# Kernel optimization log

Measured on AMD Instinct MI355X. Metric: run time of the kernel, lower is better.

The kernel has to match this reference:

```python
import jax, jax.numpy as jnp
import numpy as np

EMBED = 1024
HEADS = 16
HDIM = 64
FFN = 4 * EMBED
EPS = 1e-5


def setup_inputs() -> dict:
    key = jax.random.key(0)
    ks = jax.random.split(key, 12)
    def lin(k, fan_in, shape):
        b = 1.0 / np.sqrt(fan_in)
        return jax.random.uniform(k, shape, jnp.float32, -b, b)
    return {
        "x": jax.random.normal(ks[0], (4, 2048, EMBED), jnp.float32),
        "Wq": lin(ks[1], EMBED, (EMBED, HEADS * HDIM)),
        "Wk": lin(ks[2], EMBED, (EMBED, HEADS * HDIM)),
        "Wv": lin(ks[3], EMBED, (EMBED, HEADS * HDIM)),
        "Wo": lin(ks[4], HEADS * HDIM, (HEADS * HDIM, EMBED)),
        "ln1_g": jnp.ones((EMBED,), jnp.float32),
        "ln1_b": jnp.zeros((EMBED,), jnp.float32),
        "ln2_g": jnp.ones((EMBED,), jnp.float32),
        "ln2_b": jnp.zeros((EMBED,), jnp.float32),
        "W1": lin(ks[5], EMBED, (EMBED, FFN)),
        "b1": lin(ks[6], EMBED, (FFN,)),
        "W2": lin(ks[7], FFN, (FFN, EMBED)),
        "b2": lin(ks[8], FFN, (EMBED,)),
    }


def _layer_norm(x, g, b):
    mu = jnp.mean(x, axis=-1, keepdims=True)
    var = jnp.var(x, axis=-1, keepdims=True)
    return (x - mu) * jax.lax.rsqrt(var + EPS) * g + b


def reference(x, Wq, Wk, Wv, Wo, ln1_g, ln1_b, ln2_g, ln2_b, W1, b1, W2, b2):
    B, S, _ = x.shape
    residual = x
    h = _layer_norm(x, ln1_g, ln1_b)
    # project and split heads: [B, H, S, Dh]
    q = (h @ Wq).reshape(B, S, HEADS, HDIM).transpose(0, 2, 1, 3)
    k = (h @ Wk).reshape(B, S, HEADS, HDIM).transpose(0, 2, 1, 3)
    v = (h @ Wv).reshape(B, S, HEADS, HDIM).transpose(0, 2, 1, 3)
    scale = HDIM ** -0.5
    scores = jnp.einsum("bhqd,bhkd->bhqk", q, k) * scale
    # causal mask (upper triangle excluded above diagonal -> -inf)
    mask = jnp.triu(jnp.ones((S, S), bool), k=1)
    scores = jnp.where(mask, -jnp.inf, scores)
    attn = jax.nn.softmax(scores, axis=-1)
    out = jnp.einsum("bhqk,bhkd->bhqd", attn, v)
    out = out.transpose(0, 2, 1, 3).reshape(B, S, HEADS * HDIM)
    x = residual + out @ Wo
    residual = x
    h = _layer_norm(x, ln2_g, ln2_b)
    h = jax.nn.gelu(h @ W1 + b1, approximate=False) @ W2 + b2
    return residual + h
```

## Files before the change

### kernel.cpp

```cpp
#include <hip/hip_runtime.h>
#include <hip/hip_bf16.h>
#include <math.h>

typedef __bf16 bf16;
typedef bf16 bf16x8 __attribute__((ext_vector_type(8)));
typedef bf16 bf16x4 __attribute__((ext_vector_type(4)));
typedef float f32x4 __attribute__((ext_vector_type(4)));

#define ROWS 8192
#define EMB  1024
#define NH   16
#define HD   64
#define FFN  4096
#define QKVN 3072
#define SEQ  2048

__device__ __forceinline__ void gl2lds16(const bf16* g, bf16* l) {
  __builtin_amdgcn_global_load_lds((const __attribute__((address_space(1))) void*)g,
                                   (__attribute__((address_space(3))) void*)l, 16, 0, 0);
}

__global__ void transpose_cast(const float* __restrict__ W, bf16* __restrict__ Wt,
                               int K, int N, float scale) {
  __shared__ float tile[32][33];
  const int n0 = blockIdx.x * 32, k0 = blockIdx.y * 32;
  const int tx = threadIdx.x & 31, ty = threadIdx.x >> 5;
#pragma unroll
  for (int i = 0; i < 32; i += 8)
    tile[ty + i][tx] = W[(size_t)(k0 + ty + i) * N + n0 + tx];
  __syncthreads();
#pragma unroll
  for (int i = 0; i < 32; i += 8)
    Wt[(size_t)(n0 + ty + i) * K + k0 + tx] = (bf16)(tile[tx][ty + i] * scale);
}

__global__ void v_transpose(const bf16* __restrict__ qkv, bf16* __restrict__ vt) {
  __shared__ bf16 tile[32][33];
  const int s0 = blockIdx.x * 32, d0 = blockIdx.y * 32, bh = blockIdx.z;
  const int b = bh >> 4, h = bh & 15;
  const int tx = threadIdx.x & 31, ty = threadIdx.x >> 5;
#pragma unroll
  for (int i = 0; i < 32; i += 8)
    tile[ty + i][tx] = qkv[(size_t)(b * SEQ + s0 + ty + i) * QKVN + 2 * EMB + h * HD + d0 + tx];
  __syncthreads();
#pragma unroll
  for (int i = 0; i < 32; i += 8)
    vt[(size_t)(bh * HD + d0 + ty + i) * SEQ + s0 + tx] = tile[tx][ty + i];
}

__global__ void layernorm_bf16(const float* __restrict__ x, const float* __restrict__ g,
                               const float* __restrict__ b, bf16* __restrict__ out) {
  const int row = blockIdx.x;
  const int t = threadIdx.x;
  const float4 v = ((const float4*)(x + (size_t)row * EMB))[t];
  float s = v.x + v.y + v.z + v.w;
  float ss = v.x * v.x + v.y * v.y + v.z * v.z + v.w * v.w;
#pragma unroll
  for (int off = 32; off; off >>= 1) {
    s += __shfl_down(s, off);
    ss += __shfl_down(ss, off);
  }
  __shared__ float sbuf[8];
  const int wave = t >> 6, lane = t & 63;
  if (lane == 0) { sbuf[wave] = s; sbuf[4 + wave] = ss; }
  __syncthreads();
  if (t == 0) {
    float S = sbuf[0] + sbuf[1] + sbuf[2] + sbuf[3];
    float SS = sbuf[4] + sbuf[5] + sbuf[6] + sbuf[7];
    float mu = S * (1.0f / EMB);
    float var = SS * (1.0f / EMB) - mu * mu;
    sbuf[0] = mu;
    sbuf[1] = rsqrtf(var + 1e-5f);
  }
  __syncthreads();
  const float mu = sbuf[0], rs = sbuf[1];
  const float4 gv = ((const float4*)g)[t];
  const float4 bv = ((const float4*)b)[t];
  bf16x4 o;
  o[0] = (bf16)((v.x - mu) * rs * gv.x + bv.x);
  o[1] = (bf16)((v.y - mu) * rs * gv.y + bv.y);
  o[2] = (bf16)((v.z - mu) * rs * gv.z + bv.z);
  o[3] = (bf16)((v.w - mu) * rs * gv.w + bv.w);
  *(bf16x4*)(out + (size_t)row * EMB + t * 4) = o;
}

template <int EPI, int N_, int K_>
__global__ __launch_bounds__(256, 2) void gemm_bt(
    const bf16* __restrict__ A, const bf16* __restrict__ Bt, void* __restrict__ C,
    const float* __restrict__ bias, const float* __restrict__ resid) {
  constexpr int N = N_, K = K_;
  __shared__ __align__(16) bf16 As[128 * 64];
  __shared__ __align__(16) bf16 Bs[128 * 64];
  const int tid = threadIdx.x;
  const int lane = tid & 63;
  const int wave = tid >> 6;
  const int wm = (wave >> 1) * 64;
  const int wn = (wave & 1) * 64;
  constexpr int tn = N / 128;
  const int lin = blockIdx.y * tn + blockIdx.x;
  const int xcd = lin & 7;
  const int idx = lin >> 3;
  const int m0 = (xcd * 8 + (idx & 7)) * 128;
  const int n0 = (idx >> 3) * 128;
  const int quad = lane >> 4;
  const int l16 = lane & 15;
  const int srow8 = lane >> 3;
  const int scol = ((lane & 7) ^ srow8) * 8;
  const int xr = l16 & 7;

  const bf16* ap = A + (size_t)(m0 + wave * 32 + srow8) * K + scol;
  const bf16* bp = Bt + (size_t)(n0 + wave * 32 + srow8) * K + scol;
  bf16* const as0 = &As[wave * 32 * 64];
  bf16* const bs0 = &Bs[wave * 32 * 64];

  f32x4 acc[4][4] = {};

  for (int kt = 0; kt < K; kt += 64) {
    __syncthreads();
#pragma unroll
    for (int q = 0; q < 4; q++) {
      gl2lds16(ap + q * 8 * K, as0 + q * 8 * 64);
      gl2lds16(bp + q * 8 * K, bs0 + q * 8 * 64);
    }
    ap += 64;
    bp += 64;
    __syncthreads();
#pragma unroll
    for (int h = 0; h < 2; h++) {
      const int cp = ((h * 4 + quad) ^ xr) * 8;
      bf16x8 af[4], bfr[4];
#pragma unroll
      for (int i = 0; i < 4; i++)
        af[i] = *(const bf16x8*)&As[(wm + i * 16 + l16) * 64 + cp];
#pragma unroll
      for (int j = 0; j < 4; j++)
        bfr[j] = *(const bf16x8*)&Bs[(wn + j * 16 + l16) * 64 + cp];
#pragma unroll
      for (int i = 0; i < 4; i++)
#pragma unroll
        for (int j = 0; j < 4; j++)
          acc[i][j] = __builtin_amdgcn_mfma_f32_16x16x32_bf16(af[i], bfr[j], acc[i][j], 0, 0, 0);
    }
  }

#pragma unroll
  for (int i = 0; i < 4; i++)
#pragma unroll
    for (int j = 0; j < 4; j++)
#pragma unroll
      for (int r = 0; r < 4; r++) {
        const int row = m0 + wm + i * 16 + quad * 4 + r;
        const int col = n0 + wn + j * 16 + l16;
        const size_t idx2 = (size_t)row * N + col;
        float v = acc[i][j][r];
        if (EPI == 0) {
          ((bf16*)C)[idx2] = (bf16)v;
        } else if (EPI == 1) {
          ((float*)C)[idx2] = v + resid[idx2];
        } else if (EPI == 2) {
          v += bias[col];
          const float u = 1.5957691216f * (v + 0.044715f * v * v * v);
          v = v / (1.0f + __expf(-u));
          ((bf16*)C)[idx2] = (bf16)v;
        } else {
          ((float*)C)[idx2] = v + bias[col] + resid[idx2];
        }
      }
}

__global__ __launch_bounds__(256, 6) void flash_attn(
    const bf16* __restrict__ qkv, const bf16* __restrict__ vt, bf16* __restrict__ out) {
  const int bid = blockIdx.x;
  const int xcd = bid & 7;
  const int idx = bid >> 3;
  const int pr = idx & 15;
  const int bh = xcd + ((idx >> 4) << 3);
  const int b = bh >> 4, h = bh & 15;
  const int tid = threadIdx.x;
  const int lane = tid & 63, wave = tid >> 6;
  const int quad = lane >> 4, l16 = lane & 15;

  __shared__ __align__(16) bf16 Ks[64 * 64];
  __shared__ __align__(16) bf16 Vts[64 * 64];
  __shared__ __align__(16) bf16 Ps[4][16][72];

  const size_t rowbase = (size_t)b * SEQ;
  const int s8 = (lane >> 3) & 7;
  const int cs = ((lane & 7) ^ s8) * 8;
  const int xk = l16 & 7;
  const bf16* kbase = qkv + rowbase * QKVN + EMB + h * HD;
  const bf16* vbase = vt + (size_t)(bh * HD) * SEQ;

#pragma unroll 1
  for (int half = 0; half < 2; half++) {
    const int qt = half ? pr : 31 - pr;
    const int qrow_a = qt * 64 + wave * 16 + l16;
    const bf16* qptr = qkv + (rowbase + qrow_a) * QKVN + h * HD;
    const bf16x8 qf0 = *(const bf16x8*)(qptr + quad * 8);
    const bf16x8 qf1 = *(const bf16x8*)(qptr + 32 + quad * 8);
    f32x4 o0 = {}, o1 = {}, o2 = {}, o3 = {};
    f32x4 lsum = {};
    const int qrow_c = qt * 64 + wave * 16 + quad * 4;

    const bf16* kp = kbase + (size_t)(wave * 8 + s8) * QKVN + cs;
    const bf16* vp = vbase + (size_t)(wave * 8 + s8) * SEQ + cs;

#pragma unroll 1
    for (int kt = 0; kt <= qt; kt++) {
      __syncthreads();
      gl2lds16(kp + (size_t)kt * 64 * QKVN, &Ks[(wave * 8) * 64]);
      gl2lds16(kp + (size_t)(kt * 64 + 32) * QKVN, &Ks[(32 + wave * 8) * 64]);
      gl2lds16(vp + kt * 64, &Vts[(wave * 8) * 64]);
      gl2lds16(vp + (size_t)32 * SEQ + kt * 64, &Vts[(32 + wave * 8) * 64]);
      __syncthreads();

      if (kt < qt) {
#pragma unroll
        for (int j = 0; j < 4; j++) {
          const int rr = (j * 16 + l16) * 64;
          const bf16x8 kf0 = *(const bf16x8*)&Ks[rr + (quad ^ xk) * 8];
          const bf16x8 kf1 = *(const bf16x8*)&Ks[rr + ((4 + quad) ^ xk) * 8];
          f32x4 a = {};
          a = __builtin_amdgcn_mfma_f32_16x16x32_bf16(qf0, kf0, a, 0, 0, 0);
          a = __builtin_amdgcn_mfma_f32_16x16x32_bf16(qf1, kf1, a, 0, 0, 0);
#pragma unroll
          for (int r = 0; r < 4; r++) {
            const float pj = __expf(a[r]);
            lsum[r] += pj;
            Ps[wave][quad * 4 + r][j * 16 + l16] = (bf16)pj;
          }
        }
      } else {
#pragma unroll
        for (int j = 0; j < 4; j++) {
          if (j > wave) {
#pragma unroll
            for (int r = 0; r < 4; r++)
              Ps[wave][quad * 4 + r][j * 16 + l16] = (bf16)0.0f;
          } else {
            const int rr = (j * 16 + l16) * 64;
            const bf16x8 kf0 = *(const bf16x8*)&Ks[rr + (quad ^ xk) * 8];
            const bf16x8 kf1 = *(const bf16x8*)&Ks[rr + ((4 + quad) ^ xk) * 8];
            f32x4 a = {};
            a = __builtin_amdgcn_mfma_f32_16x16x32_bf16(qf0, kf0, a, 0, 0, 0);
            a = __builtin_amdgcn_mfma_f32_16x16x32_bf16(qf1, kf1, a, 0, 0, 0);
            if (j == wave) {
#pragma unroll
              for (int r = 0; r < 4; r++) {
                const float v = (l16 > quad * 4 + r) ? -INFINITY : a[r];
                const float pj = __expf(v);
                lsum[r] += pj;
                Ps[wave][quad * 4 + r][j * 16 + l16] = (bf16)pj;
              }
            } else {
#pragma unroll
              for (int r = 0; r < 4; r++) {
                const float pj = __expf(a[r]);
                lsum[r] += pj;
                Ps[wave][quad * 4 + r][j * 16 + l16] = (bf16)pj;
              }
            }
          }
        }
      }

      const bf16x8 af0 = *(const bf16x8*)&Ps[wave][l16][quad * 8];
      const bf16x8 af1 = *(const bf16x8*)&Ps[wave][l16][32 + quad * 8];
#pragma unroll
      for (int j = 0; j < 4; j++) {
        const int rr = (j * 16 + l16) * 64;
        const bf16x8 vf0 = *(const bf16x8*)&Vts[rr + (quad ^ xk) * 8];
        const bf16x8 vf1 = *(const bf16x8*)&Vts[rr + ((4 + quad) ^ xk) * 8];
        f32x4& oj = (j == 0) ? o0 : (j == 1) ? o1 : (j == 2) ? o2 : o3;
        oj = __builtin_amdgcn_mfma_f32_16x16x32_bf16(af0, vf0, oj, 0, 0, 0);
        oj = __builtin_amdgcn_mfma_f32_16x16x32_bf16(af1, vf1, oj, 0, 0, 0);
      }
    }

#pragma unroll
    for (int r = 0; r < 4; r++) {
      float ls = lsum[r];
      ls += __shfl_xor(ls, 1);
      ls += __shfl_xor(ls, 2);
      ls += __shfl_xor(ls, 4);
      ls += __shfl_xor(ls, 8);
      const float iv = 1.0f / ls;
      bf16* op = out + (rowbase + qrow_c + r) * EMB + h * HD;
      op[0 + l16] = (bf16)(o0[r] * iv);
      op[16 + l16] = (bf16)(o1[r] * iv);
      op[32 + l16] = (bf16)(o2[r] * iv);
      op[48 + l16] = (bf16)(o3[r] * iv);
    }
  }
}

extern "C" void kernel_launch(void* const* d_in, const int* in_sizes, int n_in,
                              void* d_out, int out_size, void* d_ws, size_t ws_size,
                              hipStream_t stream) {
  const float* x     = (const float*)d_in[0];
  const float* Wq    = (const float*)d_in[1];
  const float* Wk    = (const float*)d_in[2];
  const float* Wv    = (const float*)d_in[3];
  const float* Wo    = (const float*)d_in[4];
  const float* ln1_g = (const float*)d_in[5];
  const float* ln1_b = (const float*)d_in[6];
  const float* ln2_g = (const float*)d_in[7];
  const float* ln2_b = (const float*)d_in[8];
  const float* W1    = (const float*)d_in[9];
  const float* b1    = (const float*)d_in[10];
  const float* W2    = (const float*)d_in[11];
  const float* b2    = (const float*)d_in[12];
  float* out = (float*)d_out;

  bf16* p = (bf16*)d_ws;
  bf16* wqkv_t = p;                 p += (size_t)QKVN * EMB;
  bf16* wo_t   = p;                 p += (size_t)EMB * EMB;
  bf16* w1_t   = p;                 p += (size_t)FFN * EMB;
  bf16* w2_t   = p;                 p += (size_t)EMB * FFN;
  bf16* h      = p;                 p += (size_t)ROWS * EMB;
  bf16* qkv    = p;                 p += (size_t)ROWS * QKVN;
  bf16* attn_o = p;                 p += (size_t)ROWS * EMB;
  bf16* ffn1   = p;
  bf16* vt     = h;

  transpose_cast<<<dim3(32, 32), 256, 0, stream>>>(Wq, wqkv_t, EMB, EMB, 0.125f);
  transpose_cast<<<dim3(32, 32), 256, 0, stream>>>(Wk, wqkv_t + (size_t)EMB * EMB, EMB, EMB, 1.0f);
  transpose_cast<<<dim3(32, 32), 256, 0, stream>>>(Wv, wqkv_t + (size_t)2 * EMB * EMB, EMB, EMB, 1.0f);
  transpose_cast<<<dim3(32, 32), 256, 0, stream>>>(Wo, wo_t, EMB, EMB, 1.0f);
  transpose_cast<<<dim3(128, 32), 256, 0, stream>>>(W1, w1_t, EMB, FFN, 1.0f);
  transpose_cast<<<dim3(32, 128), 256, 0, stream>>>(W2, w2_t, FFN, EMB, 1.0f);

  layernorm_bf16<<<ROWS, 256, 0, stream>>>(x, ln1_g, ln1_b, h);

  gemm_bt<0, QKVN, EMB><<<dim3(QKVN / 128, ROWS / 128), 256, 0, stream>>>(
      h, wqkv_t, qkv, nullptr, nullptr);

  v_transpose<<<dim3(SEQ / 32, HD / 32, 64), 256, 0, stream>>>(qkv, vt);

  flash_attn<<<1024, 256, 0, stream>>>(qkv, vt, attn_o);

  gemm_bt<1, EMB, EMB><<<dim3(EMB / 128, ROWS / 128), 256, 0, stream>>>(
      attn_o, wo_t, out, nullptr, x);

  layernorm_bf16<<<ROWS, 256, 0, stream>>>(out, ln2_g, ln2_b, h);

  gemm_bt<2, FFN, EMB><<<dim3(FFN / 128, ROWS / 128), 256, 0, stream>>>(
      h, w1_t, ffn1, b1, nullptr);

  gemm_bt<3, EMB, FFN><<<dim3(EMB / 128, ROWS / 128), 256, 0, stream>>>(
      ffn1, w2_t, out, b2, out);
}
```

Before: 457.7 us.

## Replace GEMM with 8-wave double-buffered 256-row tiles and ping-pong MFMA scheduling

Swaps the 128x128 single-buffered GEMM for a 512-thread kernel using 256xBN tiles (BN 256 or 128) with double-buffered LDS and staged async global-to-LDS loads. These loads are interleaved with four MFMA phases, using barriers, s_setprio and explicit waitcnt. The aim is to hide global memory latency behind tensor work and to raise data reuse per tile. It uses more LDS and registers per block, and it relies on hand-tuned waitcnt counts that must stay correct for every config.

```diff
diff --git a/kernel.cpp b/kernel.cpp
--- a/kernel.cpp
+++ b/kernel.cpp
@@ -9,7 +9,7 @@
 
 #define ROWS 8192
 #define EMB  1024
-#define NH   16
+#define NH_  16
 #define HD   64
 #define FFN  4096
 #define QKVN 3072
@@ -84,74 +84,154 @@
   *(bf16x4*)(out + (size_t)row * EMB + t * 4) = o;
 }
 
-template <int EPI, int N_, int K_>
-__global__ __launch_bounds__(256, 2) void gemm_bt(
+template <int EPI, int N_, int K_, int BN_>
+__global__ __launch_bounds__(512, 2) void gemm8p(
     const bf16* __restrict__ A, const bf16* __restrict__ Bt, void* __restrict__ C,
     const float* __restrict__ bias, const float* __restrict__ resid) {
-  constexpr int N = N_, K = K_;
-  __shared__ __align__(16) bf16 As[128 * 64];
-  __shared__ __align__(16) bf16 Bs[128 * 64];
+  constexpr int K = K_;
+  constexpr int NF = BN_ / 64;
+  constexpr int NHF = NF / 2;
+  constexpr int WTN = BN_ / 4;
+  constexpr int BRH = BN_ / 2;
+  constexpr int BCALLS = BRH / 64;
+  constexpr int VM_N = 2 * BCALLS + 2;
+  constexpr int MT = ROWS / 256;
+  constexpr int NT = N_ / BN_;
+  constexpr int NTK = K / 64;
+  static_assert((MT * NT) % 8 == 0, "grid must split evenly over 8 XCDs");
+  static_assert(NTK >= 4 && (NTK % 2) == 0, "K-tile count must be even >=4");
+
+  __shared__ __align__(16) bf16 As[2][256 * 64];
+  __shared__ __align__(16) bf16 Bs[2][BN_ * 64];
+
   const int tid = threadIdx.x;
-  const int lane = tid & 63;
-  const int wave = tid >> 6;
-  const int wm = (wave >> 1) * 64;
-  const int wn = (wave & 1) * 64;
-  constexpr int tn = N / 128;
-  const int lin = blockIdx.y * tn + blockIdx.x;
-  const int xcd = lin & 7;
-  const int idx = lin >> 3;
-  const int m0 = (xcd * 8 + (idx & 7)) * 128;
-  const int n0 = (idx >> 3) * 128;
-  const int quad = lane >> 4;
-  const int l16 = lane & 15;
-  const int srow8 = lane >> 3;
-  const int scol = ((lane & 7) ^ srow8) * 8;
+  const int lane = tid & 63, wave = tid >> 6;
+  const int wm = wave >> 2, wn = wave & 3;
+  const int quad = lane >> 4, l16 = lane & 15;
+  const int srow = lane >> 3, ch = lane & 7;
   const int xr = l16 & 7;
 
-  const bf16* ap = A + (size_t)(m0 + wave * 32 + srow8) * K + scol;
-  const bf16* bp = Bt + (size_t)(n0 + wave * 32 + srow8) * K + scol;
-  bf16* const as0 = &As[wave * 32 * 64];
-  bf16* const bs0 = &Bs[wave * 32 * 64];
-
-  f32x4 acc[4][4] = {};
-
-  for (int kt = 0; kt < K; kt += 64) {
-    __syncthreads();
-#pragma unroll
-    for (int q = 0; q < 4; q++) {
-      gl2lds16(ap + q * 8 * K, as0 + q * 8 * 64);
-      gl2lds16(bp + q * 8 * K, bs0 + q * 8 * 64);
-    }
-    ap += 64;
-    bp += 64;
-    __syncthreads();
-#pragma unroll
-    for (int h = 0; h < 2; h++) {
-      const int cp = ((h * 4 + quad) ^ xr) * 8;
-      bf16x8 af[4], bfr[4];
-#pragma unroll
-      for (int i = 0; i < 4; i++)
-        af[i] = *(const bf16x8*)&As[(wm + i * 16 + l16) * 64 + cp];
-#pragma unroll
-      for (int j = 0; j < 4; j++)
-        bfr[j] = *(const bf16x8*)&Bs[(wn + j * 16 + l16) * 64 + cp];
-#pragma unroll
-      for (int i = 0; i < 4; i++)
-#pragma unroll
-        for (int j = 0; j < 4; j++)
-          acc[i][j] = __builtin_amdgcn_mfma_f32_16x16x32_bf16(af[i], bfr[j], acc[i][j], 0, 0, 0);
-    }
-  }
-
-#pragma unroll
-  for (int i = 0; i < 4; i++)
-#pragma unroll
-    for (int j = 0; j < 4; j++)
+  constexpr int nwg = MT * NT;
+  constexpr int cpx = nwg / 8;
+  const int lin = blockIdx.x;
+  const int wgid = (lin & 7) * cpx + (lin >> 3);
+  const int m0 = (wgid % MT) * 256;
+  const int n0 = (wgid / MT) * BN_;
+
+  const bf16* a_src = A + (size_t)(m0 + wave * 8 + srow) * K + (ch ^ srow) * 8;
+  const bf16* b_src = Bt + (size_t)(n0 + wave * 8 + srow) * K + (ch ^ srow) * 8;
+
+  f32x4 acc[8][NF] = {};
+  bf16x8 af[4][2];
+  bf16x8 bfr[NF][2];
+
+#define STAGE_A(BUF, HH, TT)                                                   \
+  {                                                                            \
+    _Pragma("unroll") for (int q = 0; q < 2; q++)                              \
+        gl2lds16(a_src + (size_t)((HH)*128 + q * 64) * K + (size_t)(TT)*64,    \
+                 &As[(BUF)][((HH)*128 + q * 64 + wave * 8) * 64]);             \
+  }
+#define STAGE_B(BUF, HH, TT)                                                   \
+  {                                                                            \
+    _Pragma("unroll") for (int q = 0; q < BCALLS; q++)                         \
+        gl2lds16(b_src + (size_t)((HH)*BRH + q * 64) * K + (size_t)(TT)*64,    \
+                 &Bs[(BUF)][((HH)*BRH + q * 64 + wave * 8) * 64]);             \
+  }
+#define DS_A(BUF, HH)                                                          \
+  {                                                                            \
+    _Pragma("unroll") for (int i = 0; i < 4; i++)                              \
+        _Pragma("unroll") for (int ks = 0; ks < 2; ks++)                       \
+            af[i][ks] = *(const bf16x8*)&As[(BUF)][                            \
+                (wm * 128 + (HH)*64 + i * 16 + l16) * 64 +                     \
+                (((ks * 4 + quad) ^ xr) * 8)];                                 \
+  }
+#define DS_B(BUF)                                                              \
+  {                                                                            \
+    _Pragma("unroll") for (int j = 0; j < NF; j++)                             \
+        _Pragma("unroll") for (int ks = 0; ks < 2; ks++)                       \
+            bfr[j][ks] = *(const bf16x8*)&Bs[(BUF)][                           \
+                (wn * WTN + j * 16 + l16) * 64 +                               \
+                (((ks * 4 + quad) ^ xr) * 8)];                                 \
+  }
+#define MMA_PH(IH, JH)                                                         \
+  {                                                                            \
+    _Pragma("unroll") for (int i = 0; i < 4; i++)                              \
+        _Pragma("unroll") for (int jj = 0; jj < NHF; jj++)                     \
+            _Pragma("unroll") for (int ks = 0; ks < 2; ks++)                   \
+                acc[(IH)*4 + i][(JH)*NHF + jj] =                               \
+                    __builtin_amdgcn_mfma_f32_16x16x32_bf16(                   \
+                        af[i][ks], bfr[(JH)*NHF + jj][ks],                     \
+                        acc[(IH)*4 + i][(JH)*NHF + jj], 0, 0, 0);              \
+  }
+#define KTILE(BUF, TT, MODE)                                                   \
+  {                                                                            \
+            \
+    DS_A(BUF, 0);                                                              \
+    DS_B(BUF);                                                                 \
+    if ((MODE) < 2) STAGE_A((BUF) ^ 1, 1, (TT) + 1);                           \
+    __builtin_amdgcn_s_barrier();                                              \
+    asm volatile("s_waitcnt lgkmcnt(0)");                                      \
+    __builtin_amdgcn_sched_barrier(0);                                         \
+    __builtin_amdgcn_s_setprio(1);                                             \
+    MMA_PH(0, 0);                                                              \
+    __builtin_amdgcn_s_setprio(0);                                             \
+    __builtin_amdgcn_s_barrier();                                              \
+                       \
+    if ((MODE) == 0) STAGE_B(BUF, 0, (TT) + 2);                                \
+    __builtin_amdgcn_s_barrier();                                              \
+    __builtin_amdgcn_s_setprio(1);                                             \
+    MMA_PH(0, 1);                                                              \
+    __builtin_amdgcn_s_setprio(0);                                             \
+    __builtin_amdgcn_s_barrier();                                              \
+                                     \
+    DS_A(BUF, 1);                                                              \
+    if ((MODE) == 0) STAGE_B(BUF, 1, (TT) + 2);                                \
+    __builtin_amdgcn_s_barrier();                                              \
+    asm volatile("s_waitcnt lgkmcnt(0)");                                      \
+    __builtin_amdgcn_sched_barrier(0);                                         \
+    __builtin_amdgcn_s_setprio(1);                                             \
+    MMA_PH(1, 0);                                                              \
+    __builtin_amdgcn_s_setprio(0);                                             \
+    __builtin_amdgcn_s_barrier();                                              \
+          \
+    if ((MODE) == 0) STAGE_A(BUF, 0, (TT) + 2);                                \
+    __builtin_amdgcn_s_barrier();                                              \
+    __builtin_amdgcn_s_setprio(1);                                             \
+    MMA_PH(1, 1);                                                              \
+    __builtin_amdgcn_s_setprio(0);                                             \
+    if ((MODE) == 0) {                                                         \
+      asm volatile("s_waitcnt vmcnt(%0)" ::"i"(VM_N));                         \
+    } else if ((MODE) == 1) {                                                  \
+      asm volatile("s_waitcnt vmcnt(0)");                                      \
+    }                                                                          \
+    __builtin_amdgcn_s_barrier();                                              \
+  }
+
+  STAGE_B(0, 0, 0); STAGE_B(0, 1, 0); STAGE_A(0, 0, 0); STAGE_A(0, 1, 0);
+  STAGE_B(1, 0, 1); STAGE_B(1, 1, 1); STAGE_A(1, 0, 1);
+  asm volatile("s_waitcnt vmcnt(%0)" ::"i"(VM_N));
+  __builtin_amdgcn_s_barrier();
+
+  for (int t = 0; t < NTK - 2; ++t) KTILE(t & 1, t, 0);
+  KTILE(0, NTK - 2, 1);
+  KTILE(1, 0, 2);
+
+#undef KTILE
+#undef MMA_PH
+#undef DS_B
+#undef DS_A
+#undef STAGE_B
+#undef STAGE_A
+
+#pragma unroll
+  for (int i = 0; i < 8; i++)
+#pragma unroll
+    for (int j = 0; j < NF; j++) {
+      const int col = n0 + wn * WTN + j * 16 + l16;
 #pragma unroll
       for (int r = 0; r < 4; r++) {
-        const int row = m0 + wm + i * 16 + quad * 4 + r;
-        const int col = n0 + wn + j * 16 + l16;
-        const size_t idx2 = (size_t)row * N + col;
+        const int row = m0 + wm * 128 + i * 16 + quad * 4 + r;
+        const size_t idx2 = (size_t)row * N_ + col;
         float v = acc[i][j][r];
         if (EPI == 0) {
           ((bf16*)C)[idx2] = (bf16)v;
@@ -166,6 +246,7 @@
           ((float*)C)[idx2] = v + bias[col] + resid[idx2];
         }
       }
+    }
 }
 
 __global__ __launch_bounds__(256, 6) void flash_attn(
@@ -332,21 +413,21 @@
 
   layernorm_bf16<<<ROWS, 256, 0, stream>>>(x, ln1_g, ln1_b, h);
 
-  gemm_bt<0, QKVN, EMB><<<dim3(QKVN / 128, ROWS / 128), 256, 0, stream>>>(
+  gemm8p<0, QKVN, EMB, 256><<<dim3((QKVN / 256) * (ROWS / 256)), 512, 0, stream>>>(
       h, wqkv_t, qkv, nullptr, nullptr);
 
   v_transpose<<<dim3(SEQ / 32, HD / 32, 64), 256, 0, stream>>>(qkv, vt);
 
   flash_attn<<<1024, 256, 0, stream>>>(qkv, vt, attn_o);
 
-  gemm_bt<1, EMB, EMB><<<dim3(EMB / 128, ROWS / 128), 256, 0, stream>>>(
+  gemm8p<1, EMB, EMB, 128><<<dim3((EMB / 128) * (ROWS / 256)), 512, 0, stream>>>(
       attn_o, wo_t, out, nullptr, x);
 
   layernorm_bf16<<<ROWS, 256, 0, stream>>>(out, ln2_g, ln2_b, h);
 
-  gemm_bt<2, FFN, EMB><<<dim3(FFN / 128, ROWS / 128), 256, 0, stream>>>(
+  gemm8p<2, FFN, EMB, 256><<<dim3((FFN / 256) * (ROWS / 256)), 512, 0, stream>>>(
       h, w1_t, ffn1, b1, nullptr);
 
-  gemm_bt<3, EMB, FFN><<<dim3(EMB / 128, ROWS / 128), 256, 0, stream>>>(
+  gemm8p<3, EMB, FFN, 128><<<dim3((EMB / 128) * (ROWS / 256)), 512, 0, stream>>>(
       ffn1, w2_t, out, b2, out);
 }
```

Result: slower. 543.5 us (+18.7%).
